# Performance work log

Measured on AMD Instinct MI355X. Metric: run time of the kernel, lower is better.

## Reference

```python
import jax, jax.numpy as jnp
import numpy as np

B, T, E, U, V = 512, 256, 256, 512, 10000


def _lstm_scan(x_seq, Wx, Wh, b, reverse=False):
    # x_seq: [B, T, E]; returns final (h, c), each [B, U]
    def step(carry, x_t):
        h, c = carry
        gates = x_t @ Wx + h @ Wh + b  # [B, 4U]
        i, f, g, o = jnp.split(gates, 4, axis=-1)
        i = jax.nn.sigmoid(i)
        f = jax.nn.sigmoid(f)
        o = jax.nn.sigmoid(o)
        g = jnp.tanh(g)
        c = f * c + i * g
        h = o * jnp.tanh(c)
        return (h, c), None

    init = (jnp.zeros((x_seq.shape[0], U), x_seq.dtype),
            jnp.zeros((x_seq.shape[0], U), x_seq.dtype))
    xs = jnp.swapaxes(x_seq, 0, 1)  # [T, B, E]
    (h, c), _ = jax.lax.scan(step, init, xs, reverse=reverse)
    return h, c


def setup_inputs() -> dict:
    key = jax.random.key(0)
    ks = jax.random.split(key, 12)
    s = lambda k, shape, scale: jax.random.normal(k, shape, jnp.float32) * scale
    return {
        "sentence": jax.random.randint(ks[0], (B, T), 0, V),
        "emb": s(ks[1], (V, E), 0.05),
        "Wx_fw": s(ks[2], (E, 4 * U), 1.0 / np.sqrt(E)),
        "Wh_fw": s(ks[3], (U, 4 * U), 1.0 / np.sqrt(U)),
        "b_fw": jnp.zeros((4 * U,), jnp.float32),
        "Wx_bw": s(ks[4], (E, 4 * U), 1.0 / np.sqrt(E)),
        "Wh_bw": s(ks[5], (U, 4 * U), 1.0 / np.sqrt(U)),
        "b_bw": jnp.zeros((4 * U,), jnp.float32),
        "W1": s(ks[6], (2 * U, 64), 1.0 / np.sqrt(2 * U)),
        "b1": jnp.zeros((64,), jnp.float32),
        "W2": s(ks[7], (64, V), 1.0 / np.sqrt(64)),
        "b2": jnp.zeros((V,), jnp.float32),
    }


def reference(sentence, emb, Wx_fw, Wh_fw, b_fw, Wx_bw, Wh_bw, b_bw, W1, b1, W2, b2):
    x = emb[sentence]  # [B, T, E]
    h_fw, _ = _lstm_scan(x, Wx_fw, Wh_fw, b_fw, reverse=False)
    # backward loop iterates t = T-1 .. 0, i.e. consumes the sequence reversed
    h_bw, _ = _lstm_scan(x, Wx_bw, Wh_bw, b_bw, reverse=True)
    h = jnp.concatenate([h_fw, h_bw], axis=-1)  # [B, 2U]
    hidden = jax.nn.relu(h @ W1 + b1)
    return jax.nn.softmax(hidden @ W2 + b2, axis=-1)
```

## Files before the change

### kernel.cpp

```cpp
#include <hip/hip_runtime.h>

#define Bb 512
#define Tt 256
#define Ee 256
#define Uu 512
#define Vv 10000

#define PACKB_OFF 0
#define HBUF_OFF  6291456
#define HID_OFF   8388608
#define CNT_OFF   8519680
#define EMB_OFF   12582912

typedef __attribute__((ext_vector_type(8))) short short8;
typedef __attribute__((ext_vector_type(4))) float f32x4;

__device__ __forceinline__ float bf2f(ushort u) {
  union { unsigned int i; float f; } v; v.i = ((unsigned int)u) << 16; return v.f;
}
__device__ __forceinline__ ushort f2bf(float f) {
  union { float f; unsigned int i; } v; v.f = f;
  unsigned int x = v.i;
  return (ushort)((x + 0x7fffu + ((x >> 16) & 1u)) >> 16);
}
__device__ __forceinline__ float fast_sigmoid(float x) {
  return 1.f / (1.f + __expf(-x));
}
__device__ __forceinline__ float fast_tanh(float x) {
  float t = __expf(-2.f * fabsf(x));
  float r = (1.f - t) / (1.f + t);
  return x >= 0.f ? r : -r;
}

__device__ __forceinline__ short8 load_h16(const ushort* p) {
  union { unsigned long long u[2]; short8 s; } v;
  v.u[0] = __hip_atomic_load((const unsigned long long*)p,     __ATOMIC_RELAXED, __HIP_MEMORY_SCOPE_AGENT);
  v.u[1] = __hip_atomic_load((const unsigned long long*)p + 1, __ATOMIC_RELAXED, __HIP_MEMORY_SCOPE_AGENT);
  return v.s;
}

__global__ __launch_bounds__(256) void init_zero(char* ob)
{
  if (blockIdx.x < 512) {
    uint4 z; z.x = 0; z.y = 0; z.z = 0; z.w = 0;
    ((uint4*)(ob + HBUF_OFF))[(size_t)blockIdx.x * 256 + threadIdx.x] = z;
  } else {
    uint2 z2; z2.x = 0; z2.y = 0;
    ((uint2*)(ob + CNT_OFF))[threadIdx.x] = z2;
  }
}

__global__ __launch_bounds__(256) void conv_emb(const float* __restrict__ emb, char* ob)
{
  ushort* embB = (ushort*)(ob + EMB_OFF);
  size_t i = ((size_t)blockIdx.x * 256 + threadIdx.x) * 8;
  f32x4 f0 = *(const f32x4*)(emb + i);
  f32x4 f1 = *(const f32x4*)(emb + i + 4);
  short8 v;
  #pragma unroll
  for (int j = 0; j < 4; j++) {
    v[j]     = (short)f2bf(f0[j]);
    v[4 + j] = (short)f2bf(f1[j]);
  }
  *(short8*)(embB + i) = v;
}

__global__ __launch_bounds__(256) void pack_weights(
    const float* __restrict__ Wx_fw, const float* __restrict__ Wh_fw,
    const float* __restrict__ Wx_bw, const float* __restrict__ Wh_bw,
    char* ob)
{
  __shared__ ushort tile[32][520];
  ushort* packB = (ushort*)(ob + PACKB_OFF);
  const int cq = blockIdx.x;
  const int ks = blockIdx.y;
  const int d  = blockIdx.z;
  const int tid = threadIdx.x;
  const float* Wx = d ? Wx_bw : Wx_fw;
  const float* Wh = d ? Wh_bw : Wh_fw;
  const int colbase = cq * 512;

  #pragma unroll
  for (int i = 0; i < 8; i++) {
    int chunk = tid + i * 256;
    int row = chunk >> 6;
    int cc = (chunk & 63) * 8;
    int k = ks * 32 + row;
    const float* src = (k < Ee) ? (Wx + (size_t)k * 2048 + colbase + cc)
                                : (Wh + (size_t)(k - Ee) * 2048 + colbase + cc);
    f32x4 f0 = *(const f32x4*)src;
    f32x4 f1 = *(const f32x4*)(src + 4);
    #pragma unroll
    for (int j = 0; j < 4; j++) {
      tile[row][cc + j]     = f2bf(f0[j]);
      tile[row][cc + 4 + j] = f2bf(f1[j]);
    }
  }
  __syncthreads();
  #pragma unroll
  for (int i = 0; i < 8; i++) {
    int chunk = tid + i * 256;
    int ctl = chunk >> 6;
    int lane = chunk & 63;
    int quad = lane >> 4, l15 = lane & 15;
    short8 v;
    #pragma unroll
    for (int jj = 0; jj < 8; jj++)
      v[jj] = (short)tile[quad * 8 + jj][ctl * 16 + l15];
    int ct = (colbase >> 4) + ctl;
    *(short8*)(packB + (((size_t)(d * 128 + ct) * 24 + ks) * 512) + lane * 8) = v;
  }
}

__global__ __launch_bounds__(256) void lstm_persistent(
    char* ob, const int* __restrict__ sent,
    const float* __restrict__ b_fw, const float* __restrict__ b_bw)
{
  __shared__ ushort ldsB[32768];
  const ushort* packB = (const ushort*)(ob + PACKB_OFF);
  const ushort* embB  = (const ushort*)(ob + EMB_OFF);
  ushort* hbuf = (ushort*)(ob + HBUF_OFF);

  const int utp = blockIdx.x;
  const int bt  = blockIdx.y;
  const int d   = blockIdx.z;
  unsigned int* cnt = (unsigned int*)(ob + CNT_OFF) + (d * 8 + bt) * 32;

  const int tid = threadIdx.x;
  const int w = tid >> 6, lane = tid & 63;
  const int l15 = lane & 15, quad = lane >> 4;
  const int mbase = bt * 64;
  const int mrow0 = mbase + w * 16;
  const int u = utp * 16 + l15;

  for (int i = 0; i < 16; i++) {
    int c = tid + i * 256;
    int lc = c & 63, qc = (c >> 6) & 3, k8 = c >> 8;
    const ushort* src = packB +
        ((size_t)(d * 128 + qc * 32 + utp) * 24 + 8 + k8) * 512 + lc * 8;
    *(short8*)&ldsB[(k8 * 4 + qc) * 512 + lc * 8] = *(const short8*)src;
  }

  const float* bias = d ? b_bw : b_fw;
  const float bi  = bias[u];
  const float bfv = bias[512 + u];
  const float bg  = bias[1024 + u];
  const float bo  = bias[1536 + u];

  const ushort* bembP[4];
  #pragma unroll
  for (int q = 0; q < 4; q++)
    bembP[q] = packB + ((size_t)(d * 128 + q * 32 + utp) * 24) * 512 + lane * 8;

  float creg[4];
  #pragma unroll
  for (int r = 0; r < 4; r++) creg[r] = 0.f;

  __syncthreads();

  for (int s = 0; s < Tt; s++) {
    const int t = d ? (Tt - 1 - s) : s;
    const ushort* hread  = hbuf + (size_t)((s & 1) * 2 + d) * Bb * Uu;
    ushort*       hwrite = hbuf + (size_t)((((s & 1) ^ 1) * 2) + d) * Bb * Uu;

    f32x4 acc[4];
    #pragma unroll
    for (int q = 0; q < 4; q++) acc[q] = (f32x4){0.f, 0.f, 0.f, 0.f};

    const int tok = sent[(mrow0 + l15) * Tt + t];
    const ushort* e0 = embB + (size_t)tok * Ee + quad * 8;

    #pragma unroll
    for (int ks = 0; ks < 8; ks++) {
      short8 a0 = *(const short8*)(e0 + ks * 32);
      short8 bq0 = *(const short8*)(bembP[0] + ks * 512);
      short8 bq1 = *(const short8*)(bembP[1] + ks * 512);
      short8 bq2 = *(const short8*)(bembP[2] + ks * 512);
      short8 bq3 = *(const short8*)(bembP[3] + ks * 512);
      acc[0] = __builtin_amdgcn_mfma_f32_16x16x32_bf16(a0, bq0, acc[0], 0, 0, 0);
      acc[1] = __builtin_amdgcn_mfma_f32_16x16x32_bf16(a0, bq1, acc[1], 0, 0, 0);
      acc[2] = __builtin_amdgcn_mfma_f32_16x16x32_bf16(a0, bq2, acc[2], 0, 0, 0);
      acc[3] = __builtin_amdgcn_mfma_f32_16x16x32_bf16(a0, bq3, acc[3], 0, 0, 0);
    }

    if (tid == 0) {
      const unsigned int target = 32u * (unsigned int)s;
      while (__hip_atomic_load(cnt, __ATOMIC_RELAXED,
                               __HIP_MEMORY_SCOPE_AGENT) < target)
        __builtin_amdgcn_s_sleep(1);
    }
    __syncthreads();

    const ushort* h0 = hread + (size_t)(mrow0 + l15) * Uu + quad * 8;
    #pragma unroll
    for (int k8 = 0; k8 < 16; k8++) {
      short8 a0 = load_h16(h0 + k8 * 32);
      short8 bq0 = *(const short8*)&ldsB[(k8 * 4 + 0) * 512 + lane * 8];
      short8 bq1 = *(const short8*)&ldsB[(k8 * 4 + 1) * 512 + lane * 8];
      short8 bq2 = *(const short8*)&ldsB[(k8 * 4 + 2) * 512 + lane * 8];
      short8 bq3 = *(const short8*)&ldsB[(k8 * 4 + 3) * 512 + lane * 8];
      acc[0] = __builtin_amdgcn_mfma_f32_16x16x32_bf16(a0, bq0, acc[0], 0, 0, 0);
      acc[1] = __builtin_amdgcn_mfma_f32_16x16x32_bf16(a0, bq1, acc[1], 0, 0, 0);
      acc[2] = __builtin_amdgcn_mfma_f32_16x16x32_bf16(a0, bq2, acc[2], 0, 0, 0);
      acc[3] = __builtin_amdgcn_mfma_f32_16x16x32_bf16(a0, bq3, acc[3], 0, 0, 0);
    }

    #pragma unroll
    for (int r = 0; r < 4; r++) {
      float iv = fast_sigmoid(acc[0][r] + bi);
      float fv = fast_sigmoid(acc[1][r] + bfv);
      float gv = fast_tanh(acc[2][r] + bg);
      float ov = fast_sigmoid(acc[3][r] + bo);
      float cn = fv * creg[r] + iv * gv;
      creg[r] = cn;
      unsigned int x = f2bf(ov * fast_tanh(cn));
      unsigned int y = (unsigned int)__shfl_xor((int)x, 1);
      unsigned int w01 = x | (y << 16);
      unsigned int w23 = (unsigned int)__shfl_xor((int)w01, 2);
      if ((l15 & 3) == 0) {
        int m = mrow0 + quad * 4 + r;
        unsigned long long v8 = ((unsigned long long)w23 << 32) | w01;
        __hip_atomic_store(
            (unsigned long long*)(hwrite + (size_t)m * Uu + utp * 16 + l15),
            v8, __ATOMIC_RELAXED, __HIP_MEMORY_SCOPE_AGENT);
      }
    }

    __syncthreads();
    if (tid == 0)
      __hip_atomic_fetch_add(cnt, 1u, __ATOMIC_RELAXED, __HIP_MEMORY_SCOPE_AGENT);
  }
}

__global__ __launch_bounds__(256) void hidden_kernel(
    char* ob, const float* __restrict__ W1, const float* __restrict__ b1)
{
  const ushort* hbuf = (const ushort*)(ob + HBUF_OFF);
  float* hidden = (float*)(ob + HID_OFF);
  int m = blockIdx.x * 4 + (threadIdx.x >> 6);
  int col = threadIdx.x & 63;
  const ushort* hf = hbuf + (size_t)m * Uu;
  const ushort* hb = hbuf + (size_t)(Bb + m) * Uu;
  float acc = b1[col];
  for (int k = 0; k < 512; k++) acc += bf2f(hf[k]) * W1[k * 64 + col];
  for (int k = 0; k < 512; k++) acc += bf2f(hb[k]) * W1[(512 + k) * 64 + col];
  hidden[(size_t)m * 64 + col] = fmaxf(acc, 0.f);
}

__device__ __forceinline__ void softmax_row(
    const float* hs, const float* __restrict__ W2, const float* __restrict__ b2,
    float* out, int m, float* red)
{
  const int tid = threadIdx.x;
  float lg[40];
  float mx = -1e30f;
  #pragma unroll 4
  for (int i = 0; i < 40; i++) {
    int c = tid + i * 256;
    float a = -1e30f;
    if (c < Vv) {
      a = b2[c];
      for (int k = 0; k < 64; k++) a += hs[k] * W2[(size_t)k * Vv + c];
    }
    lg[i] = a;
    mx = fmaxf(mx, a);
  }
  red[tid] = mx; __syncthreads();
  for (int off = 128; off > 0; off >>= 1) {
    if (tid < off) red[tid] = fmaxf(red[tid], red[tid + off]);
    __syncthreads();
  }
  mx = red[0];
  __syncthreads();

  float sum = 0.f;
  #pragma unroll 4
  for (int i = 0; i < 40; i++) {
    int c = tid + i * 256;
    if (c < Vv) { lg[i] = __expf(lg[i] - mx); sum += lg[i]; }
  }
  red[tid] = sum; __syncthreads();
  for (int off = 128; off > 0; off >>= 1) {
    if (tid < off) red[tid] += red[tid + off];
    __syncthreads();
  }
  float inv = 1.f / red[0];
  __syncthreads();
  #pragma unroll 4
  for (int i = 0; i < 40; i++) {
    int c = tid + i * 256;
    if (c < Vv) out[(size_t)m * Vv + c] = lg[i] * inv;
  }
}

__global__ __launch_bounds__(256) void logits_main(
    char* ob, const float* __restrict__ W2, const float* __restrict__ b2)
{
  __shared__ float hs[64];
  __shared__ float red[256];
  const float* hidden = (const float*)(ob + HID_OFF);
  float* out = (float*)ob;
  int bx = blockIdx.x;
  int m = (bx < 209) ? bx : (bx + 4);
  if (threadIdx.x < 64) hs[threadIdx.x] = hidden[(size_t)m * 64 + threadIdx.x];
  __syncthreads();
  softmax_row(hs, W2, b2, out, m, red);
}

__global__ __launch_bounds__(256) void logits_tail(
    char* ob, const float* __restrict__ W2, const float* __restrict__ b2)
{
  __shared__ float hs4[4][64];
  __shared__ float red[256];
  const float* hidden = (const float*)(ob + HID_OFF);
  float* out = (float*)ob;
  {
    int r = threadIdx.x >> 6, col = threadIdx.x & 63;
    hs4[r][col] = hidden[(size_t)(209 + r) * 64 + col];
  }
  __syncthreads();
  for (int r = 0; r < 4; r++) {
    softmax_row(hs4[r], W2, b2, out, 209 + r, red);
    __syncthreads();
  }
}

extern "C" void kernel_launch(void* const* d_in, const int* in_sizes, int n_in,
                              void* d_out, int out_size, void* d_ws, size_t ws_size,
                              hipStream_t stream)
{
  const int*   sent  = (const int*)d_in[0];
  const float* emb   = (const float*)d_in[1];
  const float* Wx_fw = (const float*)d_in[2];
  const float* Wh_fw = (const float*)d_in[3];
  const float* b_fw  = (const float*)d_in[4];
  const float* Wx_bw = (const float*)d_in[5];
  const float* Wh_bw = (const float*)d_in[6];
  const float* b_bw  = (const float*)d_in[7];
  const float* W1    = (const float*)d_in[8];
  const float* b1    = (const float*)d_in[9];
  const float* W2    = (const float*)d_in[10];
  const float* b2    = (const float*)d_in[11];
  char* ob = (char*)d_out;
  (void)d_ws; (void)ws_size; (void)in_sizes; (void)n_in; (void)out_size;

  init_zero<<<513, 256, 0, stream>>>(ob);
  pack_weights<<<dim3(4, 24, 2), 256, 0, stream>>>(Wx_fw, Wh_fw, Wx_bw, Wh_bw, ob);
  conv_emb<<<1250, 256, 0, stream>>>(emb, ob);

  lstm_persistent<<<dim3(32, 8, 2), 256, 0, stream>>>(ob, sent, b_fw, b_bw);

  hidden_kernel<<<128, 256, 0, stream>>>(ob, W1, b1);
  logits_main<<<508, 256, 0, stream>>>(ob, W2, b2);
  logits_tail<<<1,   256, 0, stream>>>(ob, W2, b2);
}
```

Baseline: 4.188 ms.

## Halve LSTM block count with 32-unit tiles and per-block step flags

Each persistent block now computes 32 hidden units instead of 16, keeping twice the recurrent weight slice in LDS (128KB). This halves the grid to 256 blocks, so fewer blocks take part in each step's barrier. The single shared atomic counter is replaced by per-producer flag words: each block stores its step number, and 16 threads spin-poll them without sleeping. The cost is doubled LDS and register use per block, which lowers occupancy, plus the busy-spinning.

```diff
diff --git a/kernel.cpp b/kernel.cpp
--- a/kernel.cpp
+++ b/kernel.cpp
@@ -116,7 +116,7 @@
     char* ob, const int* __restrict__ sent,
     const float* __restrict__ b_fw, const float* __restrict__ b_bw)
 {
-  __shared__ ushort ldsB[32768];
+  __shared__ ushort ldsB[65536];
   const ushort* packB = (const ushort*)(ob + PACKB_OFF);
   const ushort* embB  = (const ushort*)(ob + EMB_OFF);
   ushort* hbuf = (ushort*)(ob + HBUF_OFF);
@@ -124,37 +124,43 @@
   const int utp = blockIdx.x;
   const int bt  = blockIdx.y;
   const int d   = blockIdx.z;
-  unsigned int* cnt = (unsigned int*)(ob + CNT_OFF) + (d * 8 + bt) * 32;
+  unsigned int* flags = (unsigned int*)(ob + CNT_OFF) + (d * 8 + bt) * 32;
 
   const int tid = threadIdx.x;
   const int w = tid >> 6, lane = tid & 63;
   const int l15 = lane & 15, quad = lane >> 4;
-  const int mbase = bt * 64;
-  const int mrow0 = mbase + w * 16;
-  const int u = utp * 16 + l15;
-
-  for (int i = 0; i < 16; i++) {
+  const int mrow0 = bt * 64 + w * 16;
+
+  for (int i = 0; i < 32; i++) {
     int c = tid + i * 256;
-    int lc = c & 63, qc = (c >> 6) & 3, k8 = c >> 8;
+    int lc = c & 63, ct8 = (c >> 6) & 7, k8 = c >> 9;
     const ushort* src = packB +
-        ((size_t)(d * 128 + qc * 32 + utp) * 24 + 8 + k8) * 512 + lc * 8;
-    *(short8*)&ldsB[(k8 * 4 + qc) * 512 + lc * 8] = *(const short8*)src;
+        ((size_t)(d * 128 + (ct8 >> 1) * 32 + utp * 2 + (ct8 & 1)) * 24 + 8 + k8) * 512 + lc * 8;
+    *(short8*)&ldsB[(k8 * 8 + ct8) * 512 + lc * 8] = *(const short8*)src;
   }
 
   const float* bias = d ? b_bw : b_fw;
-  const float bi  = bias[u];
-  const float bfv = bias[512 + u];
-  const float bg  = bias[1024 + u];
-  const float bo  = bias[1536 + u];
-
-  const ushort* bembP[4];
-  #pragma unroll
-  for (int q = 0; q < 4; q++)
-    bembP[q] = packB + ((size_t)(d * 128 + q * 32 + utp) * 24) * 512 + lane * 8;
-
-  float creg[4];
-  #pragma unroll
-  for (int r = 0; r < 4; r++) creg[r] = 0.f;
+  float bi[2], bff[2], bg[2], bo[2];
+  #pragma unroll
+  for (int j = 0; j < 2; j++) {
+    int u = utp * 32 + j * 16 + l15;
+    bi[j]  = bias[u];
+    bff[j] = bias[512 + u];
+    bg[j]  = bias[1024 + u];
+    bo[j]  = bias[1536 + u];
+  }
+
+  const ushort* bembP[8];
+  #pragma unroll
+  for (int ct8 = 0; ct8 < 8; ct8++)
+    bembP[ct8] = packB +
+        ((size_t)(d * 128 + (ct8 >> 1) * 32 + utp * 2 + (ct8 & 1)) * 24) * 512 + lane * 8;
+
+  float creg[2][4];
+  #pragma unroll
+  for (int j = 0; j < 2; j++)
+    #pragma unroll
+    for (int r = 0; r < 4; r++) creg[j][r] = 0.f;
 
   __syncthreads();
 
@@ -163,9 +169,11 @@
     const ushort* hread  = hbuf + (size_t)((s & 1) * 2 + d) * Bb * Uu;
     ushort*       hwrite = hbuf + (size_t)((((s & 1) ^ 1) * 2) + d) * Bb * Uu;
 
-    f32x4 acc[4];
-    #pragma unroll
-    for (int q = 0; q < 4; q++) acc[q] = (f32x4){0.f, 0.f, 0.f, 0.f};
+    f32x4 acc[2][4];
+    #pragma unroll
+    for (int j = 0; j < 2; j++)
+      #pragma unroll
+      for (int q = 0; q < 4; q++) acc[j][q] = (f32x4){0.f, 0.f, 0.f, 0.f};
 
     const int tok = sent[(mrow0 + l15) * Tt + t];
     const ushort* e0 = embB + (size_t)tok * Ee + quad * 8;
@@ -173,21 +181,18 @@
     #pragma unroll
     for (int ks = 0; ks < 8; ks++) {
       short8 a0 = *(const short8*)(e0 + ks * 32);
-      short8 bq0 = *(const short8*)(bembP[0] + ks * 512);
-      short8 bq1 = *(const short8*)(bembP[1] + ks * 512);
-      short8 bq2 = *(const short8*)(bembP[2] + ks * 512);
-      short8 bq3 = *(const short8*)(bembP[3] + ks * 512);
-      acc[0] = __builtin_amdgcn_mfma_f32_16x16x32_bf16(a0, bq0, acc[0], 0, 0, 0);
-      acc[1] = __builtin_amdgcn_mfma_f32_16x16x32_bf16(a0, bq1, acc[1], 0, 0, 0);
-      acc[2] = __builtin_amdgcn_mfma_f32_16x16x32_bf16(a0, bq2, acc[2], 0, 0, 0);
-      acc[3] = __builtin_amdgcn_mfma_f32_16x16x32_bf16(a0, bq3, acc[3], 0, 0, 0);
-    }
-
-    if (tid == 0) {
-      const unsigned int target = 32u * (unsigned int)s;
-      while (__hip_atomic_load(cnt, __ATOMIC_RELAXED,
-                               __HIP_MEMORY_SCOPE_AGENT) < target)
-        __builtin_amdgcn_s_sleep(1);
+      #pragma unroll
+      for (int j = 0; j < 2; j++)
+        #pragma unroll
+        for (int q = 0; q < 4; q++) {
+          short8 bv = *(const short8*)(bembP[q * 2 + j] + ks * 512);
+          acc[j][q] = __builtin_amdgcn_mfma_f32_16x16x32_bf16(a0, bv, acc[j][q], 0, 0, 0);
+        }
+    }
+
+    if (tid < 16) {
+      while (__hip_atomic_load(&flags[tid], __ATOMIC_RELAXED,
+                               __HIP_MEMORY_SCOPE_AGENT) < (unsigned int)s) { }
     }
     __syncthreads();
 
@@ -195,40 +200,43 @@
     #pragma unroll
     for (int k8 = 0; k8 < 16; k8++) {
       short8 a0 = load_h16(h0 + k8 * 32);
-      short8 bq0 = *(const short8*)&ldsB[(k8 * 4 + 0) * 512 + lane * 8];
-      short8 bq1 = *(const short8*)&ldsB[(k8 * 4 + 1) * 512 + lane * 8];
-      short8 bq2 = *(const short8*)&ldsB[(k8 * 4 + 2) * 512 + lane * 8];
-      short8 bq3 = *(const short8*)&ldsB[(k8 * 4 + 3) * 512 + lane * 8];
-      acc[0] = __builtin_amdgcn_mfma_f32_16x16x32_bf16(a0, bq0, acc[0], 0, 0, 0);
-      acc[1] = __builtin_amdgcn_mfma_f32_16x16x32_bf16(a0, bq1, acc[1], 0, 0, 0);
-      acc[2] = __builtin_amdgcn_mfma_f32_16x16x32_bf16(a0, bq2, acc[2], 0, 0, 0);
-      acc[3] = __builtin_amdgcn_mfma_f32_16x16x32_bf16(a0, bq3, acc[3], 0, 0, 0);
-    }
-
-    #pragma unroll
-    for (int r = 0; r < 4; r++) {
-      float iv = fast_sigmoid(acc[0][r] + bi);
-      float fv = fast_sigmoid(acc[1][r] + bfv);
-      float gv = fast_tanh(acc[2][r] + bg);
-      float ov = fast_sigmoid(acc[3][r] + bo);
-      float cn = fv * creg[r] + iv * gv;
-      creg[r] = cn;
-      unsigned int x = f2bf(ov * fast_tanh(cn));
-      unsigned int y = (unsigned int)__shfl_xor((int)x, 1);
-      unsigned int w01 = x | (y << 16);
-      unsigned int w23 = (unsigned int)__shfl_xor((int)w01, 2);
-      if ((l15 & 3) == 0) {
-        int m = mrow0 + quad * 4 + r;
-        unsigned long long v8 = ((unsigned long long)w23 << 32) | w01;
-        __hip_atomic_store(
-            (unsigned long long*)(hwrite + (size_t)m * Uu + utp * 16 + l15),
-            v8, __ATOMIC_RELAXED, __HIP_MEMORY_SCOPE_AGENT);
+      #pragma unroll
+      for (int j = 0; j < 2; j++)
+        #pragma unroll
+        for (int q = 0; q < 4; q++) {
+          short8 bv = *(const short8*)&ldsB[(k8 * 8 + q * 2 + j) * 512 + lane * 8];
+          acc[j][q] = __builtin_amdgcn_mfma_f32_16x16x32_bf16(a0, bv, acc[j][q], 0, 0, 0);
+        }
+    }
+
+    #pragma unroll
+    for (int j = 0; j < 2; j++) {
+      #pragma unroll
+      for (int r = 0; r < 4; r++) {
+        float iv = fast_sigmoid(acc[j][0][r] + bi[j]);
+        float fv = fast_sigmoid(acc[j][1][r] + bff[j]);
+        float gv = fast_tanh(acc[j][2][r] + bg[j]);
+        float ov = fast_sigmoid(acc[j][3][r] + bo[j]);
+        float cn = fv * creg[j][r] + iv * gv;
+        creg[j][r] = cn;
+        unsigned int x = f2bf(ov * fast_tanh(cn));
+        unsigned int y = (unsigned int)__shfl_xor((int)x, 1);
+        unsigned int w01 = x | (y << 16);
+        unsigned int w23 = (unsigned int)__shfl_xor((int)w01, 2);
+        if ((l15 & 3) == 0) {
+          int m = mrow0 + quad * 4 + r;
+          unsigned long long v8 = ((unsigned long long)w23 << 32) | w01;
+          __hip_atomic_store(
+              (unsigned long long*)(hwrite + (size_t)m * Uu + utp * 32 + j * 16 + l15),
+              v8, __ATOMIC_RELAXED, __HIP_MEMORY_SCOPE_AGENT);
+        }
       }
     }
 
     __syncthreads();
     if (tid == 0)
-      __hip_atomic_fetch_add(cnt, 1u, __ATOMIC_RELAXED, __HIP_MEMORY_SCOPE_AGENT);
+      __hip_atomic_store(&flags[utp], (unsigned int)(s + 1),
+                         __ATOMIC_RELAXED, __HIP_MEMORY_SCOPE_AGENT);
   }
 }
 
@@ -348,7 +356,7 @@
   pack_weights<<<dim3(4, 24, 2), 256, 0, stream>>>(Wx_fw, Wh_fw, Wx_bw, Wh_bw, ob);
   conv_emb<<<1250, 256, 0, stream>>>(emb, ob);
 
-  lstm_persistent<<<dim3(32, 8, 2), 256, 0, stream>>>(ob, sent, b_fw, b_bw);
+  lstm_persistent<<<dim3(16, 8, 2), 256, 0, stream>>>(ob, sent, b_fw, b_bw);
 
   hidden_kernel<<<128, 256, 0, stream>>>(ob, W1, b1);
   logits_main<<<508, 256, 0, stream>>>(ob, W2, b2);
```

New measurement: 4.364 ms. +4.2%, slower.
